# Kernel optimization log

Measured on AMD Instinct MI355X. Metric: run time of the kernel, lower is better.

## Reference

```python
import jax, jax.numpy as jnp
import numpy as np

N = 2048   # nodes in the input graph
NB = 2048  # nodes in the barycenter graph
D = 128    # embedding (feature) dimension
K = 16     # number of atoms (len(size_atoms))


def cost_mat(cost_s, cost_t, p_s, p_t, tran, emb_s, emb_t):
    """Fused Gromov-Wasserstein cost matrix.

    GW structural part:  (C_s^2 p_s) 1^T + 1 (p_t^T (C_t^2)^T) - 2 C_s T C_t^T
    Fused feature part:  0.5 * squared Euclidean distance between node embeddings.
    """
    f1 = (cost_s ** 2) @ p_s                     # (N, 1)
    f2 = p_t.T @ (cost_t ** 2).T                 # (1, NB)
    cost = f1 + f2 - 2.0 * (cost_s @ tran) @ cost_t.T  # (N, NB)
    # pairwise squared Euclidean distances between embeddings
    d_emb = (jnp.sum(emb_s ** 2, axis=1, keepdims=True)
             + jnp.sum(emb_t ** 2, axis=1)[None, :]
             - 2.0 * emb_s @ emb_t.T)            # (N, NB)
    return cost + 0.5 * d_emb


def setup_inputs() -> dict:
    key = jax.random.key(0)
    k = jax.random.split(key, 6)
    graph = jax.random.uniform(k[0], (N, N), dtype=jnp.float32)
    embedding = jax.random.normal(k[1], (N, D), dtype=jnp.float32)
    prob = jnp.ones((N, 1), jnp.float32) / N           # uniform node distribution
    graph_b = jax.random.uniform(k[2], (NB, NB), dtype=jnp.float32)
    embedding_b = jax.random.normal(k[3], (NB, D), dtype=jnp.float32)
    prob_b = jnp.ones((NB, 1), jnp.float32) / NB
    t = jax.random.uniform(k[4], (N, NB), dtype=jnp.float32)
    tran = t / jnp.sum(t)                              # valid coupling-like plan (sums to 1)
    weights = jax.nn.softmax(jax.random.normal(k[5], (K,), dtype=jnp.float32))
    return {"graph": graph, "embedding": embedding, "prob": prob,
            "graph_b": graph_b, "embedding_b": embedding_b, "prob_b": prob_b,
            "tran": tran, "weights": weights, "ole_coeff": 1, "idx": 0}


def reference(graph, embedding, prob, graph_b, embedding_b, prob_b, tran, weights, ole_coeff, idx):
    # NOTE: the torch forward also computes cluster/entropy (OLE) losses from
    # `weights`, but they do NOT enter the returned value, which is only
    # <cost_mat(...), tran>. We therefore return exactly that inner product.
    cost = cost_mat(graph, graph_b, prob, prob_b, tran, embedding, embedding_b)
    return jnp.sum(cost * tran)
```

## Files before the change

kernel.cpp:

```cpp
#include <hip/hip_runtime.h>
#include <hip/hip_bf16.h>

#define NN 2048
#define DD 128

typedef unsigned short u16;
typedef unsigned int u32;
typedef __attribute__((ext_vector_type(8))) short bf16x8;
typedef __attribute__((ext_vector_type(4))) float f32x4;

__device__ __forceinline__ u16 f2bf(float f){
  u32 u = __float_as_uint(f);
  u32 r = (u + 0x7fffu + ((u >> 16) & 1u)) >> 16;
  return (u16)r;
}

__device__ __forceinline__ void gload16(const void* g, void* l){
  __builtin_amdgcn_global_load_lds(
      (const __attribute__((address_space(1))) u32*)g,
      (__attribute__((address_space(3))) u32*)l, 16, 0, 0);
}


__device__ __forceinline__ void rowpass_graph_body(
    int bid, int tid, const float* __restrict__ src, const float* __restrict__ w,
    u16* __restrict__ dst, float* __restrict__ red){
  int wid = tid >> 6, lane = tid & 63;
  int row = bid * 4 + wid;
  const float4* s4 = (const float4*)(src + (size_t)row * NN);
  float acc = 0.f;
  #pragma unroll
  for (int it = 0; it < NN / 256; ++it){
    int c4 = it * 64 + lane;
    float4 v = s4[c4];
    float4 ww = ((const float4*)w)[c4];
    acc += v.x*v.x*ww.x + v.y*v.y*ww.y + v.z*v.z*ww.z + v.w*v.w*ww.w;
    ushort4 o; o.x = f2bf(v.x); o.y = f2bf(v.y); o.z = f2bf(v.z); o.w = f2bf(v.w);
    ((ushort4*)(dst + (size_t)row * NN))[c4] = o;
  }
  #pragma unroll
  for (int off = 32; off; off >>= 1) acc += __shfl_down(acc, off);
  if (lane == 0) red[row] = acc;
}

__device__ __forceinline__ void tran_pass_body(
    int bx, int by, int t, float (*tile)[65],
    const float* __restrict__ src,
    u16* __restrict__ Tm, u16* __restrict__ Tt,
    float* __restrict__ rs, float* __restrict__ cls)
{
  int r0 = bx * 64, c0 = by * 64;
  #pragma unroll
  for (int it = 0; it < 4; ++it){
    int chunk = it * 256 + t; int r = chunk >> 4, c4 = chunk & 15;
    float4 v = ((const float4*)(src + (size_t)(r0 + r) * NN + c0))[c4];
    tile[r][c4*4+0] = v.x; tile[r][c4*4+1] = v.y;
    tile[r][c4*4+2] = v.z; tile[r][c4*4+3] = v.w;
    ushort4 o; o.x = f2bf(v.x); o.y = f2bf(v.y); o.z = f2bf(v.z); o.w = f2bf(v.w);
    ((ushort4*)(Tm + (size_t)(r0 + r) * NN + c0))[c4] = o;
  }
  __syncthreads();
  #pragma unroll
  for (int it = 0; it < 4; ++it){
    int chunk = it * 256 + t; int j = chunk >> 4, i4 = chunk & 15;
    ushort4 o;
    o.x = f2bf(tile[i4*4+0][j]); o.y = f2bf(tile[i4*4+1][j]);
    o.z = f2bf(tile[i4*4+2][j]); o.w = f2bf(tile[i4*4+3][j]);
    ((ushort4*)(Tt + (size_t)(c0 + j) * NN + r0))[i4] = o;
  }
  {
    int r = t >> 2, cq = (t & 3) * 16;
    float s = 0.f;
    #pragma unroll
    for (int c = 0; c < 16; ++c) s += tile[r][cq + c];
    s += __shfl_down(s, 2);
    s += __shfl_down(s, 1);
    if ((t & 3) == 0) atomicAdd(&rs[r0 + r], s);
  }
  {
    int c = t >> 2, rq = (t & 3) * 16;
    float s = 0.f;
    #pragma unroll
    for (int r = 0; r < 16; ++r) s += tile[rq + r][c];
    s += __shfl_down(s, 2);
    s += __shfl_down(s, 1);
    if ((t & 3) == 0) atomicAdd(&cls[c0 + c], s);
  }
}

__device__ __forceinline__ void graphb_pass_body(
    int bx, int by, int t, float (*tile)[65], float* pb,
    const float* __restrict__ src, const float* __restrict__ probb,
    u16* __restrict__ CtT, float* __restrict__ f2)
{
  int r0 = bx * 64, c0 = by * 64;
  if (t < 64) pb[t] = probb[c0 + t];
  #pragma unroll
  for (int it = 0; it < 4; ++it){
    int chunk = it * 256 + t; int r = chunk >> 4, c4 = chunk & 15;
    float4 v = ((const float4*)(src + (size_t)(r0 + r) * NN + c0))[c4];
    tile[r][c4*4+0] = v.x; tile[r][c4*4+1] = v.y;
    tile[r][c4*4+2] = v.z; tile[r][c4*4+3] = v.w;
  }
  __syncthreads();
  #pragma unroll
  for (int it = 0; it < 4; ++it){
    int chunk = it * 256 + t; int j = chunk >> 4, i4 = chunk & 15;
    ushort4 o;
    o.x = f2bf(tile[i4*4+0][j]); o.y = f2bf(tile[i4*4+1][j]);
    o.z = f2bf(tile[i4*4+2][j]); o.w = f2bf(tile[i4*4+3][j]);
    ((ushort4*)(CtT + (size_t)(c0 + j) * NN + r0))[i4] = o;
  }
  {
    int r = t >> 2, cq = (t & 3) * 16;
    float s = 0.f;
    #pragma unroll
    for (int c = 0; c < 16; ++c){ float v = tile[r][cq + c]; s += v * v * pb[cq + c]; }
    s += __shfl_down(s, 2);
    s += __shfl_down(s, 1);
    if ((t & 3) == 0) atomicAdd(&f2[r0 + r], s);
  }
}

__device__ __forceinline__ void emb_body(
    int bid, int t, const float* __restrict__ src, u16* __restrict__ dst,
    float* __restrict__ nrm){
  int rloc = t >> 5, lane32 = t & 31;
  int row = bid * 8 + rloc;
  float4 v = ((const float4*)(src + (size_t)row * DD))[lane32];
  float a = v.x*v.x + v.y*v.y + v.z*v.z + v.w*v.w;
  ushort4 o; o.x = f2bf(v.x); o.y = f2bf(v.y); o.z = f2bf(v.z); o.w = f2bf(v.w);
  ((ushort4*)(dst + (size_t)row * DD))[lane32] = o;
  #pragma unroll
  for (int off = 16; off; off >>= 1) a += __shfl_down(a, off, 32);
  if (lane32 == 0) nrm[row] = a;
}

__global__ __launch_bounds__(256) void k_prep(
    const float* __restrict__ graph,  const float* __restrict__ prob,
    const float* __restrict__ tran,   const float* __restrict__ graphb,
    const float* __restrict__ probb,  const float* __restrict__ emb,
    const float* __restrict__ embb,
    u16* Cs, u16* Tm, u16* Tt, u16* CtT, u16* es, u16* et,
    float* f1, float* f2, float* rs, float* cls, float* ss, float* st)
{
  __shared__ float tile[64][65];
  __shared__ float pb[64];
  int b = blockIdx.x, t = threadIdx.x;
  if (b < 512){
    rowpass_graph_body(b, t, graph, prob, Cs, f1);
  } else if (b < 1536){
    int b2 = b - 512;  tran_pass_body(b2 & 31, b2 >> 5, t, tile, tran, Tm, Tt, rs, cls);
  } else if (b < 2560){
    int b2 = b - 1536; graphb_pass_body(b2 & 31, b2 >> 5, t, tile, pb, graphb, probb, CtT, f2);
  } else if (b < 2816){
    emb_body(b - 2560, t, emb, es, ss);
  } else {
    emb_body(b - 2816, t, embb, et, st);
  }
}

__global__ __launch_bounds__(512, 2) void k_gw(
    const u16* __restrict__ Cs, const u16* __restrict__ Tt,
    const u16* __restrict__ Tm, const u16* __restrict__ CtT,
    float* __restrict__ accs)
{
  __shared__ u16 lds[2][4][8192];
  const int tid = threadIdx.x;
  const int bid = blockIdx.x;
  const int swz = (bid & 7) * 32 + (bid >> 3);
  const int bi = swz >> 4, bk = swz & 15;

  const u16* srcs[4] = {Cs, Tt, Tm, CtT};
  const int panels[4] = {bi * 128, bk * 128, bi * 128, bk * 128};

  const int w = tid >> 6, lane = tid & 63;
  const int l15 = lane & 15, g = lane >> 4;
  const int gsel = w >> 2, wg = w & 3, wr = wg >> 1, wc = wg & 1;

  const int s_row = tid >> 3;
  const int s_gslot = (tid & 7) ^ (s_row & 7);

  f32x4 acc[4][4];
  #pragma unroll
  for (int m = 0; m < 4; ++m)
    #pragma unroll
    for (int n = 0; n < 4; ++n)
      acc[m][n] = (f32x4){0.f, 0.f, 0.f, 0.f};

  int offA[4][2], offB[4][2];
  #pragma unroll
  for (int m = 0; m < 4; ++m){
    int row = wr * 64 + m * 16 + l15;
    int rowb = wc * 64 + m * 16 + l15;
    #pragma unroll
    for (int kk = 0; kk < 2; ++kk){
      offA[m][kk] = row * 64 + ((((kk << 2) | g)) ^ (row & 7)) * 8;
      offB[m][kk] = rowb * 64 + ((((kk << 2) | g)) ^ (rowb & 7)) * 8;
    }
  }

  auto stage = [&](int buf, int kt){
    const size_t col = (size_t)kt * 64 + s_gslot * 8;
    #pragma unroll
    for (int tt = 0; tt < 4; ++tt){
      gload16(srcs[tt] + (size_t)(panels[tt] + s_row) * NN + col,
              &lds[buf][tt][w * 512]);
      gload16(srcs[tt] + (size_t)(panels[tt] + s_row + 64) * NN + col,
              &lds[buf][tt][4096 + w * 512]);
    }
  };

  const int NT = NN / 64;
  stage(0, 0);
  stage(1, 1);
  for (int kt = 0; kt < NT; ++kt){
    int cur = kt & 1;
    asm volatile("s_waitcnt vmcnt(8)" ::: "memory");
    __builtin_amdgcn_s_barrier();

    const u16* tA = &lds[cur][gsel * 2][0];
    const u16* tB = &lds[cur][gsel * 2 + 1][0];
    bf16x8 av[4][2], bv[4][2];
    #pragma unroll
    for (int kk = 0; kk < 2; ++kk){
      #pragma unroll
      for (int m = 0; m < 4; ++m) av[m][kk] = *(const bf16x8*)(tA + offA[m][kk]);
      #pragma unroll
      for (int n = 0; n < 4; ++n) bv[n][kk] = *(const bf16x8*)(tB + offB[n][kk]);
    }
    asm volatile("s_waitcnt lgkmcnt(0)" ::: "memory");
    __builtin_amdgcn_sched_barrier(0);
    __builtin_amdgcn_s_barrier();

    int kn = (kt + 2 < NT) ? (kt + 2) : (NT - 1);
    stage(cur, kn);

    #pragma unroll
    for (int kk = 0; kk < 2; ++kk)
      #pragma unroll
      for (int m = 0; m < 4; ++m)
        #pragma unroll
        for (int n = 0; n < 4; ++n)
          acc[m][n] = __builtin_amdgcn_mfma_f32_16x16x32_bf16(av[m][kk], bv[n][kk], acc[m][n], 0, 0, 0);
  }

  __syncthreads();

  float* ustash = (float*)&lds[0][0][0];
  if (gsel == 0){
    #pragma unroll
    for (int m = 0; m < 4; ++m)
      #pragma unroll
      for (int n = 0; n < 4; ++n)
        #pragma unroll
        for (int r = 0; r < 4; ++r){
          int row = wr * 64 + m * 16 + g * 4 + r;
          int col = wc * 64 + n * 16 + l15;
          ustash[row * 128 + col] = acc[m][n][r];
        }
  }
  __syncthreads();
  if (gsel == 1){
    float part = 0.f;
    #pragma unroll
    for (int m = 0; m < 4; ++m)
      #pragma unroll
      for (int n = 0; n < 4; ++n)
        #pragma unroll
        for (int r = 0; r < 4; ++r){
          int row = wr * 64 + m * 16 + g * 4 + r;
          int col = wc * 64 + n * 16 + l15;
          part += acc[m][n][r] * ustash[row * 128 + col];
        }
    #pragma unroll
    for (int off = 32; off; off >>= 1) part += __shfl_down(part, off);
    if (lane == 0) atomicAdd(&accs[0], part);
  }
}

__global__ __launch_bounds__(256, 2) void k_embdot(
    const u16* __restrict__ es, const u16* __restrict__ et,
    const float* __restrict__ tran,
    const float* __restrict__ f1, const float* __restrict__ f2,
    const float* __restrict__ rs, const float* __restrict__ cls,
    const float* __restrict__ ss, const float* __restrict__ st,
    float* __restrict__ accs, u32* __restrict__ ctr, float* __restrict__ out)
{
  __shared__ u16 lds[2][16384];
  __shared__ unsigned flagS;
  const int tid = threadIdx.x;
  const int bid = blockIdx.x;
  const int swz = (bid & 7) * 32 + (bid >> 3);
  const int bi = swz >> 4, bj = swz & 15;
  const int w = tid >> 6, lane = tid & 63;
  const int l15 = lane & 15, g = lane >> 4;
  const int wr = w >> 1, wc = w & 1;

  const u16* srcs[2] = {es, et};
  const int panels[2] = {bi * 128, bj * 128};

  #pragma unroll
  for (int tt = 0; tt < 2; ++tt){
    #pragma unroll
    for (int it = 0; it < 8; ++it){
      int chunk = w * 8 + it;
      int r = chunk * 4 + g;
      int s = l15 ^ (r & 15);
      gload16(srcs[tt] + (size_t)(panels[tt] + r) * DD + s * 8,
              &lds[tt][chunk * 512]);
    }
  }
  __syncthreads();

  f32x4 acc[4][4];
  #pragma unroll
  for (int m = 0; m < 4; ++m)
    #pragma unroll
    for (int n = 0; n < 4; ++n)
      acc[m][n] = (f32x4){0.f, 0.f, 0.f, 0.f};

  #pragma unroll
  for (int ks = 0; ks < 4; ++ks){
    bf16x8 av[4], bv[4];
    #pragma unroll
    for (int m = 0; m < 4; ++m){
      int row = wr * 64 + m * 16 + l15;
      int sp = (ks * 4 + g) ^ (row & 15);
      av[m] = *(const bf16x8*)((const char*)&lds[0][0] + row * 256 + sp * 16);
    }
    #pragma unroll
    for (int n = 0; n < 4; ++n){
      int rowb = wc * 64 + n * 16 + l15;
      int spb = (ks * 4 + g) ^ (rowb & 15);
      bv[n] = *(const bf16x8*)((const char*)&lds[1][0] + rowb * 256 + spb * 16);
    }
    #pragma unroll
    for (int m = 0; m < 4; ++m)
      #pragma unroll
      for (int n = 0; n < 4; ++n)
        acc[m][n] = __builtin_amdgcn_mfma_f32_16x16x32_bf16(av[m], bv[n], acc[m][n], 0, 0, 0);
  }

  float part = 0.f;
  #pragma unroll
  for (int m = 0; m < 4; ++m)
    #pragma unroll
    for (int n = 0; n < 4; ++n)
      #pragma unroll
      for (int r = 0; r < 4; ++r){
        int row = bi * 128 + wr * 64 + m * 16 + g * 4 + r;
        int col = bj * 128 + wc * 64 + n * 16 + l15;
        part += tran[(size_t)row * NN + col] * acc[m][n][r];
      }
  #pragma unroll
  for (int off = 32; off; off >>= 1) part += __shfl_down(part, off);
  if (lane == 0) atomicAdd(&accs[1], part);

  __syncthreads();
  if (tid == 0){
    __threadfence();
    unsigned d = atomicAdd(ctr, 1u);
    flagS = (d == 255u) ? 1u : 0u;
  }
  __syncthreads();
  if (flagS){
    __threadfence();
    float* red = (float*)&lds[0][0];
    float p2 = 0.f;
    for (int i = tid; i < NN; i += 256){
      p2 += (f1[i] + 0.5f * ss[i]) * rs[i];
      p2 += (f2[i] + 0.5f * st[i]) * cls[i];
    }
    red[tid] = p2; __syncthreads();
    for (int s = 128; s; s >>= 1){
      if (tid < s) red[tid] += red[tid + s];
      __syncthreads();
    }
    if (tid == 0) out[0] = red[0] - 2.0f * accs[0] - accs[1];
  }
}

extern "C" void kernel_launch(void* const* d_in, const int* in_sizes, int n_in,
                              void* d_out, int out_size, void* d_ws, size_t ws_size,
                              hipStream_t stream)
{
  const float* graph  = (const float*)d_in[0];
  const float* emb    = (const float*)d_in[1];
  const float* prob   = (const float*)d_in[2];
  const float* graphb = (const float*)d_in[3];
  const float* embb   = (const float*)d_in[4];
  const float* probb  = (const float*)d_in[5];
  const float* tran   = (const float*)d_in[6];
  (void)in_sizes; (void)n_in; (void)out_size; (void)ws_size;

  char* ws = (char*)d_ws;
  u16* Cs   = (u16*)(ws + 0);
  u16* Tm   = (u16*)(ws + 8388608);
  u16* Tt   = (u16*)(ws + 16777216);
  u16* CtT  = (u16*)(ws + 25165824);
  u16* es   = (u16*)(ws + 33554432);
  u16* et   = (u16*)(ws + 34078720);
  float* f1   = (float*)(ws + 34603008);
  float* f2   = (float*)(ws + 34611200);
  float* rs   = (float*)(ws + 34619392);
  float* cls  = (float*)(ws + 34627584);
  float* ss   = (float*)(ws + 34635776);
  float* st   = (float*)(ws + 34643968);
  float* accs = (float*)(ws + 34652160);
  u32*   ctr  = (u32*)(ws + 34652192);

  hipMemsetAsync(ws + 34603008, 0, 49216, stream);

  k_prep<<<3072, 256, 0, stream>>>(graph, prob, tran, graphb, probb, emb, embb,
                                   Cs, Tm, Tt, CtT, es, et,
                                   f1, f2, rs, cls, ss, st);
  k_gw<<<256, 512, 0, stream>>>(Cs, Tt, Tm, CtT, accs);
  k_embdot<<<256, 256, 0, stream>>>(es, et, tran, f1, f2, rs, cls, ss, st,
                                    accs, ctr, (float*)d_out);
}
```

Measured before the change: 96.10 us.

## Split GW tile GEMM pair across two blocks with bf16 partial exchange

```diff
diff --git a/kernel.cpp b/kernel.cpp
--- a/kernel.cpp
+++ b/kernel.cpp
@@ -13,6 +13,9 @@
   u32 u = __float_as_uint(f);
   u32 r = (u + 0x7fffu + ((u >> 16) & 1u)) >> 16;
   return (u16)r;
+}
+__device__ __forceinline__ float bf2f(u16 b){
+  return __uint_as_float(((u32)b) << 16);
 }
 
 __device__ __forceinline__ void gload16(const void* g, void* l){
@@ -160,6 +163,132 @@
   }
 }
 
+__global__ __launch_bounds__(256, 2) void k_gw2(
+    const u16* __restrict__ Cs, const u16* __restrict__ Tt,
+    const u16* __restrict__ Tm, const u16* __restrict__ CtT,
+    u16* __restrict__ parts,
+    u32* __restrict__ pctr, float* __restrict__ accs)
+{
+  __shared__ u16 lds[2][2][8192];
+  __shared__ unsigned flagS;
+  const int tid = threadIdx.x;
+  const int bid = blockIdx.x;
+  const int tile = bid >> 1, role = bid & 1;
+  const int swz = (tile & 7) * 32 + (tile >> 3);
+  const int bi = swz >> 4, bk = swz & 15;
+
+  const u16* Asrc = role ? Tm : Cs;
+  const u16* Bsrc = role ? CtT : Tt;
+
+  const int w = tid >> 6, lane = tid & 63;
+  const int l15 = lane & 15, g = lane >> 4;
+  const int wr = w >> 1, wc = w & 1;
+
+  const int s_row = tid >> 3;
+  const int s_gslot = (tid & 7) ^ (s_row & 7);
+
+  f32x4 acc[4][4];
+  #pragma unroll
+  for (int m = 0; m < 4; ++m)
+    #pragma unroll
+    for (int n = 0; n < 4; ++n)
+      acc[m][n] = (f32x4){0.f, 0.f, 0.f, 0.f};
+
+  int offA[4][2], offB[4][2];
+  #pragma unroll
+  for (int m = 0; m < 4; ++m){
+    int row = wr * 64 + m * 16 + l15;
+    int rowb = wc * 64 + m * 16 + l15;
+    #pragma unroll
+    for (int kk = 0; kk < 2; ++kk){
+      offA[m][kk] = row * 64 + ((((kk << 2) | g)) ^ (row & 7)) * 8;
+      offB[m][kk] = rowb * 64 + ((((kk << 2) | g)) ^ (rowb & 7)) * 8;
+    }
+  }
+
+  auto stage = [&](int buf, int kt){
+    const size_t col = (size_t)kt * 64 + s_gslot * 8;
+    #pragma unroll
+    for (int j = 0; j < 4; ++j){
+      gload16(Asrc + (size_t)(bi * 128 + s_row + j * 32) * NN + col,
+              &lds[buf][0][w * 512 + j * 2048]);
+      gload16(Bsrc + (size_t)(bk * 128 + s_row + j * 32) * NN + col,
+              &lds[buf][1][w * 512 + j * 2048]);
+    }
+  };
+
+  const int NT = NN / 64;
+  stage(0, 0);
+  stage(1, 1);
+  for (int kt = 0; kt < NT; ++kt){
+    int cur = kt & 1;
+    asm volatile("s_waitcnt vmcnt(8)" ::: "memory");
+    __builtin_amdgcn_s_barrier();
+
+    const u16* tA = &lds[cur][0][0];
+    const u16* tB = &lds[cur][1][0];
+    bf16x8 av[4][2], bv[4][2];
+    #pragma unroll
+    for (int kk = 0; kk < 2; ++kk){
+      #pragma unroll
+      for (int m = 0; m < 4; ++m) av[m][kk] = *(const bf16x8*)(tA + offA[m][kk]);
+      #pragma unroll
+      for (int n = 0; n < 4; ++n) bv[n][kk] = *(const bf16x8*)(tB + offB[n][kk]);
+    }
+    asm volatile("s_waitcnt lgkmcnt(0)" ::: "memory");
+    __builtin_amdgcn_sched_barrier(0);
+    __builtin_amdgcn_s_barrier();
+
+    int kn = (kt + 2 < NT) ? (kt + 2) : (NT - 1);
+    stage(cur, kn);
+
+    #pragma unroll
+    for (int kk = 0; kk < 2; ++kk)
+      #pragma unroll
+      for (int m = 0; m < 4; ++m)
+        #pragma unroll
+        for (int n = 0; n < 4; ++n)
+          acc[m][n] = __builtin_amdgcn_mfma_f32_16x16x32_bf16(av[m][kk], bv[n][kk], acc[m][n], 0, 0, 0);
+  }
+
+  u16* mypart = parts + (size_t)role * 4194304 + (size_t)tile * 16384;
+  #pragma unroll
+  for (int m = 0; m < 4; ++m)
+    #pragma unroll
+    for (int n = 0; n < 4; ++n)
+      #pragma unroll
+      for (int r = 0; r < 4; ++r){
+        int row = wr * 64 + m * 16 + g * 4 + r;
+        int col = wc * 64 + n * 16 + l15;
+        mypart[row * 128 + col] = f2bf(acc[m][n][r]);
+      }
+  __threadfence();
+  __syncthreads();
+  if (tid == 0){
+    u32 d = atomicAdd(&pctr[tile], 1u);
+    flagS = (d == 1u) ? 1u : 0u;
+  }
+  __syncthreads();
+  if (flagS){
+    __threadfence();
+    const u16* pp = parts + (size_t)(1 - role) * 4194304 + (size_t)tile * 16384;
+    float part = 0.f;
+    #pragma unroll
+    for (int m = 0; m < 4; ++m)
+      #pragma unroll
+      for (int n = 0; n < 4; ++n)
+        #pragma unroll
+        for (int r = 0; r < 4; ++r){
+          int row = wr * 64 + m * 16 + g * 4 + r;
+          int col = wc * 64 + n * 16 + l15;
+          part += acc[m][n][r] * bf2f(pp[row * 128 + col]);
+        }
+    #pragma unroll
+    for (int off = 32; off; off >>= 1) part += __shfl_down(part, off);
+    if (lane == 0) atomicAdd(&accs[0], part);
+  }
+}
+
 __global__ __launch_bounds__(512, 2) void k_gw(
     const u16* __restrict__ Cs, const u16* __restrict__ Tt,
     const u16* __restrict__ Tm, const u16* __restrict__ CtT,
@@ -392,7 +521,7 @@
   const float* embb   = (const float*)d_in[4];
   const float* probb  = (const float*)d_in[5];
   const float* tran   = (const float*)d_in[6];
-  (void)in_sizes; (void)n_in; (void)out_size; (void)ws_size;
+  (void)in_sizes; (void)n_in; (void)out_size;
 
   char* ws = (char*)d_ws;
   u16* Cs   = (u16*)(ws + 0);
@@ -409,13 +538,21 @@
   float* st   = (float*)(ws + 34643968);
   float* accs = (float*)(ws + 34652160);
   u32*   ctr  = (u32*)(ws + 34652192);
-
-  hipMemsetAsync(ws + 34603008, 0, 49216, stream);
+  u32*   pctr = (u32*)(ws + 34652224);
+  u16*   parts= (u16*)(ws + 34653248);
+
+  const bool split = ws_size >= 51430464ull;
+
+  hipMemsetAsync(ws + 34603008, 0, 50240, stream);
 
   k_prep<<<3072, 256, 0, stream>>>(graph, prob, tran, graphb, probb, emb, embb,
                                    Cs, Tm, Tt, CtT, es, et,
                                    f1, f2, rs, cls, ss, st);
-  k_gw<<<256, 512, 0, stream>>>(Cs, Tt, Tm, CtT, accs);
+  if (split){
+    k_gw2<<<512, 256, 0, stream>>>(Cs, Tt, Tm, CtT, parts, pctr, accs);
+  } else {
+    k_gw<<<256, 512, 0, stream>>>(Cs, Tt, Tm, CtT, accs);
+  }
   k_embdot<<<256, 256, 0, stream>>>(es, et, tran, f1, f2, rs, cls, ss, st,
                                     accs, ctr, (float*)d_out);
 }
```

After: 185.7 us. 93.2% more time.
